# Optimization experiments

Measured on AMD Instinct MI355X. Metric: run time of the kernel, lower is better.

The kernel has to match this reference:

```python
import jax, jax.numpy as jnp
import numpy as np

NUM_HEADS = 8


def setup_inputs() -> dict:
    key = jax.random.key(0)
    ks = jax.random.split(key, 9)
    B, T, N, D = 8, 12, 307, 512
    scale = 0.02
    return {
        "query": jax.random.normal(ks[0], (B, T, N, D), dtype=jnp.float32),
        "key": jax.random.normal(ks[1], (B, T, N, D), dtype=jnp.float32),
        "value": jax.random.normal(ks[2], (B, T, N, D), dtype=jnp.float32),
        "semantic_matrix": jax.random.normal(ks[3], (N, N), dtype=jnp.float32),
        "Wq": jax.random.normal(ks[4], (D, D), dtype=jnp.float32) * scale,
        "bq": jnp.zeros((D,), dtype=jnp.float32),
        "Wk": jax.random.normal(ks[5], (D, D), dtype=jnp.float32) * scale,
        "bk": jnp.zeros((D,), dtype=jnp.float32),
        "Wv": jax.random.normal(ks[6], (D, D), dtype=jnp.float32) * scale,
        "bv": jnp.zeros((D,), dtype=jnp.float32),
        "Wo": jax.random.normal(ks[7], (D, D), dtype=jnp.float32) * scale,
        "bo": jnp.zeros((D,), dtype=jnp.float32),
    }


def reference(query, key, value, semantic_matrix, Wq, bq, Wk, bk, Wv, bv, Wo, bo):
    B, T, N, D = query.shape
    H = NUM_HEADS
    hd = D // H
    # multiplicative spatial mask: row-softmax of the semantic matrix (same for all b, h, t)
    mask = jax.nn.softmax(semantic_matrix, axis=-1)  # [N, N]
    q = (query @ Wq + bq).reshape(B, T, N, H, hd)
    k = (key @ Wk + bk).reshape(B, T, N, H, hd)
    v = (value @ Wv + bv).reshape(B, T, N, H, hd)
    # attention over the node axis, per (batch, head, time step)
    scores = jnp.einsum("btnhd,btmhd->bhtnm", q, k) * (1.0 / (hd ** 0.5))  # [B,H,T,N,N]
    scores = scores * mask  # elementwise multiplicative mask (NOT additive bias)
    w = jax.nn.softmax(scores, axis=-1)
    out = jnp.einsum("bhtnm,btmhd->btnhd", w, v).reshape(B, T, N, D)
    return out @ Wo + bo
```

## Files before the change

kernel.cpp:

```cpp
#include <hip/hip_runtime.h>

#define NNODES 307
#define NPAD 320
#define HEADS 8
#define HDV 64
#define DM 512
#define BATCH 8
#define TSTEPS 12
#define MROWS (BATCH*TSTEPS*NNODES)

typedef unsigned short u16;
typedef __attribute__((ext_vector_type(8))) short s16x8;
typedef __attribute__((ext_vector_type(8))) unsigned short u16x8;
typedef __attribute__((ext_vector_type(4))) float f32x4;

__device__ __forceinline__ u16 f2bf(float f){
  unsigned int u = __builtin_bit_cast(unsigned int, f);
  u += 0x7fffu + ((u >> 16) & 1u);
  return (u16)(u >> 16);
}
__device__ __forceinline__ unsigned f2bf2(float lo, float hi){
  return (unsigned)f2bf(lo) | ((unsigned)f2bf(hi) << 16);
}
__device__ __forceinline__ void glds16(const void* g, void* l){
  __builtin_amdgcn_global_load_lds((const __attribute__((address_space(1))) void*)g,
                                   (__attribute__((address_space(3))) void*)l, 16, 0, 0);
}

struct PrepArgs { const float* w[4]; u16* o[4]; };

__global__ __launch_bounds__(256)
void prep_w(PrepArgs a){
  const float* w = a.w[blockIdx.z];
  u16* o = a.o[blockIdx.z];
  __shared__ float tile[32][33];
  int bx = blockIdx.x*32, by = blockIdx.y*32;
  int tx = threadIdx.x, ty = threadIdx.y;
  for (int i = ty; i < 32; i += 8)
    tile[i][tx] = w[(size_t)(by+i)*DM + bx + tx];
  __syncthreads();
  for (int i = ty; i < 32; i += 8)
    o[(size_t)(bx+i)*DM + by + tx] = f2bf(tile[tx][i]);
}

__global__ __launch_bounds__(256)
void mask_softmax(const float* __restrict__ sem, float* __restrict__ maskp){
  int n = blockIdx.x;
  int tid = threadIdx.x, lane = tid & 63, wid = tid >> 6;
  if (n >= NNODES){
    maskp[(size_t)n*NPAD + tid] = 0.f;
    if (tid + 256 < NPAD) maskp[(size_t)n*NPAD + tid + 256] = 0.f;
    return;
  }
  __shared__ float red[4];
  float v0 = sem[(size_t)n*NNODES + tid];
  float v1 = (tid + 256 < NNODES) ? sem[(size_t)n*NNODES + tid + 256] : -INFINITY;
  float mx = fmaxf(v0, v1);
  for (int d = 1; d < 64; d <<= 1) mx = fmaxf(mx, __shfl_xor(mx, d));
  if (lane == 0) red[wid] = mx;
  __syncthreads();
  mx = fmaxf(fmaxf(red[0], red[1]), fmaxf(red[2], red[3]));
  __syncthreads();
  float e0 = __expf(v0 - mx);
  float e1 = (tid + 256 < NNODES) ? __expf(v1 - mx) : 0.f;
  float s = e0 + e1;
  for (int d = 1; d < 64; d <<= 1) s += __shfl_xor(s, d);
  if (lane == 0) red[wid] = s;
  __syncthreads();
  s = red[0] + red[1] + red[2] + red[3];
  float rs = 0.125f / s;
  maskp[(size_t)n*NPAD + tid] = e0 * rs;
  int c2 = tid + 256;
  if (c2 < NNODES)      maskp[(size_t)n*NPAD + c2] = e1 * rs;
  else if (c2 < NPAD)   maskp[(size_t)n*NPAD + c2] = 0.f;
}

struct GemmSet { const void* A; const u16* W; const float* bias; void* C; };
struct GemmArgs { GemmSet s[3]; };

template<int AF32, int CBF16>
__global__ __launch_bounds__(256)
void gemm512(GemmArgs ga, int M){
  GemmSet g = ga.s[blockIdx.y];
  __shared__ u16 As[128*64];
  __shared__ u16 Bs[128*64];
  const int tid = threadIdx.x;
  const int lane = tid & 63;
  const int wid = tid >> 6;

  int bid = blockIdx.x;
  const int qch = 924 >> 3, rch = 924 & 7;
  int xcd = bid & 7, idx = bid >> 3;
  int wg = (xcd < rch ? xcd*(qch+1) : rch*(qch+1) + (xcd-rch)*qch) + idx;
  const int m0 = (wg >> 2) * 128;
  const int n0 = (wg & 3) * 128;
  const int wr = (wid >> 1) * 64;
  const int wc = (wid & 1) * 64;

  const f32x4 fz = {0.f, 0.f, 0.f, 0.f};
  f32x4 acc[4][4];
#pragma unroll
  for (int i = 0; i < 4; i++)
#pragma unroll
    for (int j = 0; j < 4; j++) acc[i][j] = fz;

  const int rL = (wid << 5) + (lane >> 3);
  const int cswz = (lane & 7) ^ (rL & 7);
  const u16* bsrc = g.W + (size_t)(n0 + rL)*DM + cswz*8;
  const u16* asrcB = AF32 ? nullptr : ((const u16*)g.A + (size_t)(m0 + rL)*DM + cswz*8);

  const int sr = tid >> 1;
  const int shf = tid & 1;
  const int grA = m0 + sr;
  const bool okA = grA < M;

  for (int k0 = 0; k0 < 512; k0 += 64) {
#pragma unroll
    for (int e = 0; e < 4; e++)
      glds16(bsrc + (size_t)e*8*DM + k0, Bs + (wid << 11) + (e << 9));
    if constexpr (AF32) {
      const float* src = (const float*)g.A + (size_t)grA*DM + k0 + shf*32;
      u16x8 ch[4];
#pragma unroll
      for (int i = 0; i < 4; i++) {
        float4 f0 = okA ? ((const float4*)src)[2*i]   : make_float4(0.f,0.f,0.f,0.f);
        float4 f1 = okA ? ((const float4*)src)[2*i+1] : make_float4(0.f,0.f,0.f,0.f);
        u16x8 u;
        u[0]=f2bf(f0.x); u[1]=f2bf(f0.y); u[2]=f2bf(f0.z); u[3]=f2bf(f0.w);
        u[4]=f2bf(f1.x); u[5]=f2bf(f1.y); u[6]=f2bf(f1.z); u[7]=f2bf(f1.w);
        ch[i] = u;
      }
#pragma unroll
      for (int i = 0; i < 4; i++) {
        int slot = (shf*64 + i*16) ^ ((sr & 7) << 4);
        *(u16x8*)((char*)As + sr*128 + slot) = ch[i];
      }
    } else {
#pragma unroll
      for (int e = 0; e < 4; e++)
        glds16(asrcB + (size_t)e*8*DM + k0, As + (wid << 11) + (e << 9));
    }
    __syncthreads();
    __builtin_amdgcn_s_setprio(1);
#pragma unroll
    for (int kt = 0; kt < 2; kt++) {
      int kbyte = kt*64 + (lane >> 4)*16;
      s16x8 a[4], b[4];
#pragma unroll
      for (int i = 0; i < 4; i++) {
        int row = wr + i*16 + (lane & 15);
        a[i] = *(const s16x8*)((const char*)As + row*128 + (kbyte ^ ((row & 7) << 4)));
      }
#pragma unroll
      for (int j = 0; j < 4; j++) {
        int row = wc + j*16 + (lane & 15);
        b[j] = *(const s16x8*)((const char*)Bs + row*128 + (kbyte ^ ((row & 7) << 4)));
      }
#pragma unroll
      for (int i = 0; i < 4; i++)
#pragma unroll
        for (int j = 0; j < 4; j++)
          acc[i][j] = __builtin_amdgcn_mfma_f32_16x16x32_bf16(a[i], b[j], acc[i][j], 0, 0, 0);
    }
    __builtin_amdgcn_s_setprio(0);
    __syncthreads();
  }

#pragma unroll
  for (int j = 0; j < 4; j++) {
    int gcol = n0 + wc + j*16 + (lane & 15);
    float bv = g.bias[gcol];
#pragma unroll
    for (int i = 0; i < 4; i++) {
#pragma unroll
      for (int r = 0; r < 4; r++) {
        int grow = m0 + wr + i*16 + (lane >> 4)*4 + r;
        if (grow < M) {
          float v = acc[i][j][r] + bv;
          if constexpr (CBF16) ((u16*)g.C)[(size_t)grow*DM + gcol] = f2bf(v);
          else                 ((float*)g.C)[(size_t)grow*DM + gcol] = v;
        }
      }
    }
  }
}

__global__ __launch_bounds__(640, 3)
void attn_kernel(const u16* __restrict__ Qb, const u16* __restrict__ Kb,
                 const u16* __restrict__ Vb, const float* __restrict__ maskp,
                 u16* __restrict__ attnb){
  __shared__ u16 kw[NPAD*64];
  __shared__ u16 vt[64*NPAD];
  __shared__ u16 pb[10*2*16*40];
  const int tid = threadIdx.x;
  const int lane = tid & 63;
  const int wid = tid >> 6;
  const int qq = lane & 15;
  const int gg = lane >> 4;
  const int bth = blockIdx.x;
  const int h   = bth & 7;
  const int bt  = bth >> 3;
  const size_t base = (size_t)bt * NNODES;

  const u16x8 zu = {0,0,0,0,0,0,0,0};
  const s16x8 zs = {0,0,0,0,0,0,0,0};
  const f32x4 fz = {0.f,0.f,0.f,0.f};

  s16x8 qf[2][2];
#pragma unroll
  for (int s = 0; s < 2; s++) {
    int qt = wid*2 + s;
    int qrow = qt*16 + qq;
    if (qrow < NNODES) {
      const u16* qp = Qb + (base + qrow)*DM + h*HDV + gg*8;
      qf[s][0] = *(const s16x8*)(qp);
      qf[s][1] = *(const s16x8*)(qp + 32);
    } else { qf[s][0] = zs; qf[s][1] = zs; }
  }

  for (int i = tid; i < NPAD*8; i += 640) {
    int r = i >> 3, c = i & 7;
    u16x8 kv = zu, vv = zu;
    if (r < NNODES) {
      kv = *(const u16x8*)(Kb + (base + r)*DM + h*HDV + c*8);
      vv = *(const u16x8*)(Vb + (base + r)*DM + h*HDV + c*8);
    }
    *(u16x8*)((char*)kw + r*128 + ((c*16) ^ ((r & 7) << 4))) = kv;
#pragma unroll
    for (int j = 0; j < 8; j++) {
      int d = c*8 + j;
      *(u16*)((char*)vt + d*640 + ((r*2) ^ ((d & 7) << 4))) = vv[j];
    }
  }
  __syncthreads();

  u16* pbw = pb + wid*1280;

#pragma unroll
  for (int s = 0; s < 2; s++) {
    const int qt = wid*2 + s;
    const int n = qt*16 + qq;

    f32x4 sc[20];
#pragma unroll
    for (int t = 0; t < 20; t++) sc[t] = fz;
    __builtin_amdgcn_s_setprio(1);
#pragma unroll
    for (int t = 0; t < 20; t++) {
      int m = t*16 + qq;
#pragma unroll
      for (int kt = 0; kt < 2; kt++) {
        s16x8 kf = *(const s16x8*)((const char*)kw + m*128 + ((kt*64 + gg*16) ^ ((m & 7) << 4)));
        sc[t] = __builtin_amdgcn_mfma_f32_16x16x32_bf16(kf, qf[s][kt], sc[t], 0, 0, 0);
      }
    }
    __builtin_amdgcn_s_setprio(0);

    const float* mrow = maskp + (size_t)n*NPAD + gg*4;
#pragma unroll
    for (int t = 0; t < 20; t++) {
      float4 mk = *(const float4*)(mrow + t*16);
      sc[t][0] *= mk.x; sc[t][1] *= mk.y; sc[t][2] *= mk.z; sc[t][3] *= mk.w;
    }
#pragma unroll
    for (int r = 0; r < 4; r++)
      if (304 + gg*4 + r >= NNODES) sc[19][r] = -1e30f;

    float mx = -1e30f;
#pragma unroll
    for (int t = 0; t < 20; t++)
      mx = fmaxf(fmaxf(fmaxf(mx, sc[t][0]), fmaxf(sc[t][1], sc[t][2])), sc[t][3]);
    mx = fmaxf(mx, __shfl_xor(mx, 16));
    mx = fmaxf(mx, __shfl_xor(mx, 32));

    float sum = 0.f;
#pragma unroll
    for (int t = 0; t < 20; t++) {
#pragma unroll
      for (int r = 0; r < 4; r++) { float e = __expf(sc[t][r] - mx); sc[t][r] = e; sum += e; }
    }
    sum += __shfl_xor(sum, 16);
    sum += __shfl_xor(sum, 32);
    const float rinv = 1.f / sum;

    f32x4 o[4];
#pragma unroll
    for (int dt = 0; dt < 4; dt++) o[dt] = fz;
#pragma unroll
    for (int kt = 0; kt < 10; kt++) {
      u16* ps = pbw + (kt & 1)*640;
      uint2 w0, w1;
      w0.x = f2bf2(sc[2*kt][0]*rinv,   sc[2*kt][1]*rinv);
      w0.y = f2bf2(sc[2*kt][2]*rinv,   sc[2*kt][3]*rinv);
      w1.x = f2bf2(sc[2*kt+1][0]*rinv, sc[2*kt+1][1]*rinv);
      w1.y = f2bf2(sc[2*kt+1][2]*rinv, sc[2*kt+1][3]*rinv);
      *(uint2*)(ps + qq*40 + gg*4)      = w0;
      *(uint2*)(ps + qq*40 + 16 + gg*4) = w1;
      s16x8 pa = *(const s16x8*)(ps + qq*40 + gg*8);
      __builtin_amdgcn_s_setprio(1);
#pragma unroll
      for (int dt = 0; dt < 4; dt++) {
        int d = dt*16 + qq;
        s16x8 vb = *(const s16x8*)((const char*)vt + d*640 + ((kt*64 + gg*16) ^ ((d & 7) << 4)));
        o[dt] = __builtin_amdgcn_mfma_f32_16x16x32_bf16(pa, vb, o[dt], 0, 0, 0);
      }
      __builtin_amdgcn_s_setprio(0);
    }

#pragma unroll
    for (int dt = 0; dt < 4; dt++) {
#pragma unroll
      for (int r = 0; r < 4; r++) {
        int nn = qt*16 + gg*4 + r;
        if (nn < NNODES)
          attnb[(base + nn)*DM + h*HDV + dt*16 + qq] = f2bf(o[dt][r]);
      }
    }
  }
}

extern "C" void kernel_launch(void* const* d_in, const int* in_sizes, int n_in,
                              void* d_out, int out_size, void* d_ws, size_t ws_size,
                              hipStream_t stream) {
  const float* query = (const float*)d_in[0];
  const float* key   = (const float*)d_in[1];
  const float* value = (const float*)d_in[2];
  const float* sem   = (const float*)d_in[3];
  const float* Wq = (const float*)d_in[4];
  const float* bq = (const float*)d_in[5];
  const float* Wk = (const float*)d_in[6];
  const float* bk = (const float*)d_in[7];
  const float* Wv = (const float*)d_in[8];
  const float* bv = (const float*)d_in[9];
  const float* Wo = (const float*)d_in[10];
  const float* bo = (const float*)d_in[11];
  float* out = (float*)d_out;

  char* ws = (char*)d_ws;
  size_t off = 0;
  auto alloc = [&](size_t b) { size_t o = off; off += (b + 255) & ~(size_t)255; return o; };
  float* maskp = (float*)(ws + alloc((size_t)NPAD*NPAD*4));
  u16* wtq = (u16*)(ws + alloc((size_t)DM*DM*2));
  u16* wtk = (u16*)(ws + alloc((size_t)DM*DM*2));
  u16* wtv = (u16*)(ws + alloc((size_t)DM*DM*2));
  u16* wto = (u16*)(ws + alloc((size_t)DM*DM*2));
  u16* ab = (u16*)(ws + alloc((size_t)MROWS*DM*2));
  u16* qb = (u16*)(ws + alloc((size_t)MROWS*DM*2));
  u16* kb = (u16*)(ws + alloc((size_t)MROWS*DM*2));
  u16* vb = (u16*)(ws + alloc((size_t)MROWS*DM*2));
  if (off > ws_size) return;

  PrepArgs pa;
  pa.w[0] = Wq; pa.w[1] = Wk; pa.w[2] = Wv; pa.w[3] = Wo;
  pa.o[0] = wtq; pa.o[1] = wtk; pa.o[2] = wtv; pa.o[3] = wto;
  prep_w<<<dim3(16,16,4), dim3(32,8,1), 0, stream>>>(pa);

  mask_softmax<<<dim3(NPAD), dim3(256), 0, stream>>>(sem, maskp);

  GemmArgs g3;
  g3.s[0] = { query, wtq, bq, qb };
  g3.s[1] = { key,   wtk, bk, kb };
  g3.s[2] = { value, wtv, bv, vb };
  gemm512<1,1><<<dim3(924, 3), dim3(256), 0, stream>>>(g3, MROWS);

  attn_kernel<<<dim3(BATCH*TSTEPS*HEADS), dim3(640), 0, stream>>>(qb, kb, vb, maskp, ab);

  GemmArgs g1;
  g1.s[0] = { ab, wto, bo, out };
  g1.s[1] = g1.s[0];
  g1.s[2] = g1.s[0];
  gemm512<0,0><<<dim3(924, 1), dim3(256), 0, stream>>>(g1, MROWS);
}
```

Before: 509.5 us.

## Double-buffer GEMM K loop, stage bf16 epilogue via LDS, split attention into query-tile blocks

```diff
diff --git a/kernel.cpp b/kernel.cpp
--- a/kernel.cpp
+++ b/kernel.cpp
@@ -82,11 +82,11 @@
 __global__ __launch_bounds__(256)
 void gemm512(GemmArgs ga, int M){
   GemmSet g = ga.s[blockIdx.y];
-  __shared__ u16 As[128*64];
-  __shared__ u16 Bs[128*64];
+  __shared__ u16 lds[32768];
   const int tid = threadIdx.x;
   const int lane = tid & 63;
   const int wid = tid >> 6;
+  const int qq = lane & 15, gg = lane >> 4;
 
   int bid = blockIdx.x;
   const int qch = 924 >> 3, rch = 924 & 7;
@@ -107,54 +107,60 @@
   const int rL = (wid << 5) + (lane >> 3);
   const int cswz = (lane & 7) ^ (rL & 7);
   const u16* bsrc = g.W + (size_t)(n0 + rL)*DM + cswz*8;
-  const u16* asrcB = AF32 ? nullptr : ((const u16*)g.A + (size_t)(m0 + rL)*DM + cswz*8);
+  const u16* asrcB = (const u16*)g.A + (size_t)(m0 + rL)*DM + cswz*8;
+  const int ldst = (wid << 11);
 
   const int sr = tid >> 1;
   const int shf = tid & 1;
-  const int grA = m0 + sr;
-  const bool okA = grA < M;
-
-  for (int k0 = 0; k0 < 512; k0 += 64) {
+  const float* aptr = (const float*)g.A + (size_t)(m0 + sr)*DM + shf*32;
+  const bool okA = (m0 + sr) < M;
+
+  auto stageB = [&](int c, int k0){
+    u16* dst = lds + c*16384 + 8192 + ldst;
 #pragma unroll
     for (int e = 0; e < 4; e++)
-      glds16(bsrc + (size_t)e*8*DM + k0, Bs + (wid << 11) + (e << 9));
-    if constexpr (AF32) {
-      const float* src = (const float*)g.A + (size_t)grA*DM + k0 + shf*32;
-      u16x8 ch[4];
+      glds16(bsrc + (size_t)(e*8)*DM + k0, dst + (e << 9));
+  };
+  auto stageAg = [&](int c, int k0){
+    u16* dst = lds + c*16384 + ldst;
+#pragma unroll
+    for (int e = 0; e < 4; e++)
+      glds16(asrcB + (size_t)(e*8)*DM + k0, dst + (e << 9));
+  };
+  auto loadA = [&](float4* An, int k0){
+#pragma unroll
+    for (int i = 0; i < 8; i++)
+      An[i] = okA ? ((const float4*)(aptr + k0))[i] : make_float4(0.f,0.f,0.f,0.f);
+  };
+  auto writeA = [&](const float4* An, int c){
+    u16* Abuf = lds + c*16384;
+#pragma unroll
+    for (int i = 0; i < 4; i++) {
+      float4 f0 = An[2*i], f1 = An[2*i+1];
+      u16x8 u;
+      u[0]=f2bf(f0.x); u[1]=f2bf(f0.y); u[2]=f2bf(f0.z); u[3]=f2bf(f0.w);
+      u[4]=f2bf(f1.x); u[5]=f2bf(f1.y); u[6]=f2bf(f1.z); u[7]=f2bf(f1.w);
+      int slot = (shf*64 + i*16) ^ ((sr & 7) << 4);
+      *(u16x8*)((char*)Abuf + sr*128 + slot) = u;
+    }
+  };
+  auto compute = [&](int c){
+    const char* Abuf = (const char*)(lds + c*16384);
+    const char* Bbuf = Abuf + 16384;
+    __builtin_amdgcn_s_setprio(1);
+#pragma unroll
+    for (int kt = 0; kt < 2; kt++) {
+      int kbyte = kt*64 + gg*16;
+      s16x8 a[4], b[4];
 #pragma unroll
       for (int i = 0; i < 4; i++) {
-        float4 f0 = okA ? ((const float4*)src)[2*i]   : make_float4(0.f,0.f,0.f,0.f);
-        float4 f1 = okA ? ((const float4*)src)[2*i+1] : make_float4(0.f,0.f,0.f,0.f);
-        u16x8 u;
-        u[0]=f2bf(f0.x); u[1]=f2bf(f0.y); u[2]=f2bf(f0.z); u[3]=f2bf(f0.w);
-        u[4]=f2bf(f1.x); u[5]=f2bf(f1.y); u[6]=f2bf(f1.z); u[7]=f2bf(f1.w);
-        ch[i] = u;
-      }
-#pragma unroll
-      for (int i = 0; i < 4; i++) {
-        int slot = (shf*64 + i*16) ^ ((sr & 7) << 4);
-        *(u16x8*)((char*)As + sr*128 + slot) = ch[i];
-      }
-    } else {
-#pragma unroll
-      for (int e = 0; e < 4; e++)
-        glds16(asrcB + (size_t)e*8*DM + k0, As + (wid << 11) + (e << 9));
-    }
-    __syncthreads();
-    __builtin_amdgcn_s_setprio(1);
-#pragma unroll
-    for (int kt = 0; kt < 2; kt++) {
-      int kbyte = kt*64 + (lane >> 4)*16;
-      s16x8 a[4], b[4];
-#pragma unroll
-      for (int i = 0; i < 4; i++) {
-        int row = wr + i*16 + (lane & 15);
-        a[i] = *(const s16x8*)((const char*)As + row*128 + (kbyte ^ ((row & 7) << 4)));
+        int row = wr + i*16 + qq;
+        a[i] = *(const s16x8*)(Abuf + row*128 + (kbyte ^ ((row & 7) << 4)));
       }
 #pragma unroll
       for (int j = 0; j < 4; j++) {
-        int row = wc + j*16 + (lane & 15);
-        b[j] = *(const s16x8*)((const char*)Bs + row*128 + (kbyte ^ ((row & 7) << 4)));
+        int row = wc + j*16 + qq;
+        b[j] = *(const s16x8*)(Bbuf + row*128 + (kbyte ^ ((row & 7) << 4)));
       }
 #pragma unroll
       for (int i = 0; i < 4; i++)
@@ -163,158 +169,204 @@
           acc[i][j] = __builtin_amdgcn_mfma_f32_16x16x32_bf16(a[i], b[j], acc[i][j], 0, 0, 0);
     }
     __builtin_amdgcn_s_setprio(0);
+  };
+
+  float4 An[8];
+  if constexpr (AF32) { loadA(An, 0); stageB(0, 0); writeA(An, 0); }
+  else { stageAg(0, 0); stageB(0, 0); }
+  __syncthreads();
+
+#pragma unroll
+  for (int t = 0; t < 8; t++) {
+    const int cur = t & 1;
+    if (t < 7) {
+      if constexpr (AF32) loadA(An, (t+1)*64);
+      else stageAg(cur^1, (t+1)*64);
+      stageB(cur^1, (t+1)*64);
+    }
+    compute(cur);
+    if constexpr (AF32) { if (t < 7) writeA(An, cur^1); }
     __syncthreads();
   }
 
-#pragma unroll
-  for (int j = 0; j < 4; j++) {
-    int gcol = n0 + wc + j*16 + (lane & 15);
-    float bv = g.bias[gcol];
-#pragma unroll
-    for (int i = 0; i < 4; i++) {
-#pragma unroll
-      for (int r = 0; r < 4; r++) {
-        int grow = m0 + wr + i*16 + (lane >> 4)*4 + r;
-        if (grow < M) {
-          float v = acc[i][j][r] + bv;
-          if constexpr (CBF16) ((u16*)g.C)[(size_t)grow*DM + gcol] = f2bf(v);
-          else                 ((float*)g.C)[(size_t)grow*DM + gcol] = v;
+  if constexpr (CBF16) {
+    u16* ct = lds;
+#pragma unroll
+    for (int j = 0; j < 4; j++) {
+      float bv = g.bias[n0 + wc + j*16 + qq];
+#pragma unroll
+      for (int i = 0; i < 4; i++)
+#pragma unroll
+        for (int r = 0; r < 4; r++)
+          ct[(wr + i*16 + gg*4 + r)*136 + wc + j*16 + qq] = f2bf(acc[i][j][r] + bv);
+    }
+    __syncthreads();
+#pragma unroll
+    for (int it = 0; it < 8; it++) {
+      int i = tid + it*256;
+      int row = i >> 4, seg = i & 15;
+      if (m0 + row < M)
+        *(u16x8*)((u16*)g.C + (size_t)(m0+row)*DM + n0 + seg*8) =
+            *(const u16x8*)(ct + row*136 + seg*8);
+    }
+  } else {
+#pragma unroll
+    for (int j = 0; j < 4; j++) {
+      int gcol = n0 + wc + j*16 + qq;
+      float bv = g.bias[gcol];
+#pragma unroll
+      for (int i = 0; i < 4; i++)
+#pragma unroll
+        for (int r = 0; r < 4; r++) {
+          int grow = m0 + wr + i*16 + gg*4 + r;
+          if (grow < M) ((float*)g.C)[(size_t)grow*DM + gcol] = acc[i][j][r] + bv;
         }
-      }
     }
   }
 }
 
-__global__ __launch_bounds__(640, 3)
+__global__ __launch_bounds__(256, 3)
 void attn_kernel(const u16* __restrict__ Qb, const u16* __restrict__ Kb,
                  const u16* __restrict__ Vb, const float* __restrict__ maskp,
                  u16* __restrict__ attnb){
-  __shared__ u16 kw[NPAD*64];
-  __shared__ u16 vt[64*NPAD];
-  __shared__ u16 pb[10*2*16*40];
+  __shared__ u16 kw[160*64];
+  __shared__ u16 vt[64*192];
+  __shared__ u16 pb[4*16*40];
   const int tid = threadIdx.x;
   const int lane = tid & 63;
   const int wid = tid >> 6;
   const int qq = lane & 15;
   const int gg = lane >> 4;
-  const int bth = blockIdx.x;
+  const int qt = blockIdx.x * 4 + wid;
+  const int bth = blockIdx.y;
   const int h   = bth & 7;
   const int bt  = bth >> 3;
   const size_t base = (size_t)bt * NNODES;
+  const int n = qt*16 + qq;
 
   const u16x8 zu = {0,0,0,0,0,0,0,0};
   const s16x8 zs = {0,0,0,0,0,0,0,0};
   const f32x4 fz = {0.f,0.f,0.f,0.f};
 
-  s16x8 qf[2][2];
-#pragma unroll
-  for (int s = 0; s < 2; s++) {
-    int qt = wid*2 + s;
-    int qrow = qt*16 + qq;
-    if (qrow < NNODES) {
-      const u16* qp = Qb + (base + qrow)*DM + h*HDV + gg*8;
-      qf[s][0] = *(const s16x8*)(qp);
-      qf[s][1] = *(const s16x8*)(qp + 32);
-    } else { qf[s][0] = zs; qf[s][1] = zs; }
-  }
-
-  for (int i = tid; i < NPAD*8; i += 640) {
-    int r = i >> 3, c = i & 7;
-    u16x8 kv = zu, vv = zu;
-    if (r < NNODES) {
-      kv = *(const u16x8*)(Kb + (base + r)*DM + h*HDV + c*8);
-      vv = *(const u16x8*)(Vb + (base + r)*DM + h*HDV + c*8);
-    }
-    *(u16x8*)((char*)kw + r*128 + ((c*16) ^ ((r & 7) << 4))) = kv;
-#pragma unroll
-    for (int j = 0; j < 8; j++) {
-      int d = c*8 + j;
-      *(u16*)((char*)vt + d*640 + ((r*2) ^ ((d & 7) << 4))) = vv[j];
-    }
-  }
-  __syncthreads();
-
-  u16* pbw = pb + wid*1280;
-
-#pragma unroll
-  for (int s = 0; s < 2; s++) {
-    const int qt = wid*2 + s;
-    const int n = qt*16 + qq;
-
-    f32x4 sc[20];
-#pragma unroll
-    for (int t = 0; t < 20; t++) sc[t] = fz;
+  s16x8 qf[2];
+  if (n < NNODES) {
+    const u16* qp = Qb + (base + n)*DM + h*HDV + gg*8;
+    qf[0] = *(const s16x8*)(qp);
+    qf[1] = *(const s16x8*)(qp + 32);
+  } else { qf[0] = zs; qf[1] = zs; }
+
+  f32x4 o[4] = {fz, fz, fz, fz};
+  float m_run = -1e30f, l_run = 0.f;
+  u16* pbw = pb + wid*640;
+
+  for (int hf = 0; hf < 2; hf++) {
+    for (int i = tid; i < 160*8; i += 256) {
+      int rl = i >> 3, c = i & 7, gr = hf*160 + rl;
+      u16x8 kv = zu, vv = zu;
+      if (gr < NNODES) {
+        kv = *(const u16x8*)(Kb + (base + gr)*DM + h*HDV + c*8);
+        vv = *(const u16x8*)(Vb + (base + gr)*DM + h*HDV + c*8);
+      }
+      *(u16x8*)((char*)kw + rl*128 + ((c*16) ^ ((rl & 7) << 4))) = kv;
+#pragma unroll
+      for (int j = 0; j < 8; j++) {
+        int d = c*8 + j;
+        *(u16*)((char*)vt + d*384 + ((rl*2) ^ ((d & 7) << 4))) = vv[j];
+      }
+    }
+    __syncthreads();
+
+    f32x4 sc[10];
+#pragma unroll
+    for (int t = 0; t < 10; t++) sc[t] = fz;
     __builtin_amdgcn_s_setprio(1);
 #pragma unroll
-    for (int t = 0; t < 20; t++) {
-      int m = t*16 + qq;
+    for (int t = 0; t < 10; t++) {
+      int ml = t*16 + qq;
 #pragma unroll
       for (int kt = 0; kt < 2; kt++) {
-        s16x8 kf = *(const s16x8*)((const char*)kw + m*128 + ((kt*64 + gg*16) ^ ((m & 7) << 4)));
-        sc[t] = __builtin_amdgcn_mfma_f32_16x16x32_bf16(kf, qf[s][kt], sc[t], 0, 0, 0);
+        s16x8 kf = *(const s16x8*)((const char*)kw + ml*128 + ((kt*64 + gg*16) ^ ((ml & 7) << 4)));
+        sc[t] = __builtin_amdgcn_mfma_f32_16x16x32_bf16(kf, qf[kt], sc[t], 0, 0, 0);
       }
     }
     __builtin_amdgcn_s_setprio(0);
 
-    const float* mrow = maskp + (size_t)n*NPAD + gg*4;
-#pragma unroll
-    for (int t = 0; t < 20; t++) {
+    const float* mrow = maskp + (size_t)n*NPAD + hf*160 + gg*4;
+#pragma unroll
+    for (int t = 0; t < 10; t++) {
       float4 mk = *(const float4*)(mrow + t*16);
       sc[t][0] *= mk.x; sc[t][1] *= mk.y; sc[t][2] *= mk.z; sc[t][3] *= mk.w;
     }
-#pragma unroll
-    for (int r = 0; r < 4; r++)
-      if (304 + gg*4 + r >= NNODES) sc[19][r] = -1e30f;
-
-    float mx = -1e30f;
-#pragma unroll
-    for (int t = 0; t < 20; t++)
-      mx = fmaxf(fmaxf(fmaxf(mx, sc[t][0]), fmaxf(sc[t][1], sc[t][2])), sc[t][3]);
-    mx = fmaxf(mx, __shfl_xor(mx, 16));
-    mx = fmaxf(mx, __shfl_xor(mx, 32));
-
+    if (hf) {
+#pragma unroll
+      for (int r = 0; r < 4; r++)
+        if (304 + gg*4 + r >= NNODES) sc[9][r] = -1e30f;
+    }
+
+    float mh = -1e30f;
+#pragma unroll
+    for (int t = 0; t < 10; t++)
+      mh = fmaxf(fmaxf(fmaxf(mh, sc[t][0]), fmaxf(sc[t][1], sc[t][2])), sc[t][3]);
+    mh = fmaxf(mh, __shfl_xor(mh, 16));
+    mh = fmaxf(mh, __shfl_xor(mh, 32));
+    float mnew = fmaxf(m_run, mh);
+    float scl = __expf(m_run - mnew);
+    m_run = mnew;
     float sum = 0.f;
 #pragma unroll
-    for (int t = 0; t < 20; t++) {
-#pragma unroll
-      for (int r = 0; r < 4; r++) { float e = __expf(sc[t][r] - mx); sc[t][r] = e; sum += e; }
+    for (int t = 0; t < 10; t++) {
+#pragma unroll
+      for (int r = 0; r < 4; r++) { float e = __expf(sc[t][r] - mnew); sc[t][r] = e; sum += e; }
     }
     sum += __shfl_xor(sum, 16);
     sum += __shfl_xor(sum, 32);
-    const float rinv = 1.f / sum;
-
-    f32x4 o[4];
-#pragma unroll
-    for (int dt = 0; dt < 4; dt++) o[dt] = fz;
-#pragma unroll
-    for (int kt = 0; kt < 10; kt++) {
-      u16* ps = pbw + (kt & 1)*640;
+    l_run = l_run * scl + sum;
+    float srs[4];
+#pragma unroll
+    for (int r = 0; r < 4; r++) srs[r] = __shfl(scl, gg*4 + r);
+#pragma unroll
+    for (int dt = 0; dt < 4; dt++) {
+      o[dt][0] *= srs[0]; o[dt][1] *= srs[1]; o[dt][2] *= srs[2]; o[dt][3] *= srs[3];
+    }
+
+#pragma unroll
+    for (int kt = 0; kt < 5; kt++) {
       uint2 w0, w1;
-      w0.x = f2bf2(sc[2*kt][0]*rinv,   sc[2*kt][1]*rinv);
-      w0.y = f2bf2(sc[2*kt][2]*rinv,   sc[2*kt][3]*rinv);
-      w1.x = f2bf2(sc[2*kt+1][0]*rinv, sc[2*kt+1][1]*rinv);
-      w1.y = f2bf2(sc[2*kt+1][2]*rinv, sc[2*kt+1][3]*rinv);
-      *(uint2*)(ps + qq*40 + gg*4)      = w0;
-      *(uint2*)(ps + qq*40 + 16 + gg*4) = w1;
-      s16x8 pa = *(const s16x8*)(ps + qq*40 + gg*8);
+      w0.x = f2bf2(sc[2*kt][0],   sc[2*kt][1]);
+      w0.y = f2bf2(sc[2*kt][2],   sc[2*kt][3]);
+      w1.x = f2bf2(sc[2*kt+1][0], sc[2*kt+1][1]);
+      w1.y = f2bf2(sc[2*kt+1][2], sc[2*kt+1][3]);
+      *(uint2*)(pbw + qq*40 + gg*4)      = w0;
+      *(uint2*)(pbw + qq*40 + 16 + gg*4) = w1;
+      s16x8 pa = *(const s16x8*)(pbw + qq*40 + gg*8);
       __builtin_amdgcn_s_setprio(1);
 #pragma unroll
       for (int dt = 0; dt < 4; dt++) {
         int d = dt*16 + qq;
-        s16x8 vb = *(const s16x8*)((const char*)vt + d*640 + ((kt*64 + gg*16) ^ ((d & 7) << 4)));
-        o[dt] = __builtin_amdgcn_mfma_f32_16x16x32_bf16(pa, vb, o[dt], 0, 0, 0);
+        s16x8 vbf = *(const s16x8*)((const char*)vt + d*384 + ((kt*64 + gg*16) ^ ((d & 7) << 4)));
+        o[dt] = __builtin_amdgcn_mfma_f32_16x16x32_bf16(pa, vbf, o[dt], 0, 0, 0);
       }
       __builtin_amdgcn_s_setprio(0);
     }
-
-#pragma unroll
-    for (int dt = 0; dt < 4; dt++) {
-#pragma unroll
-      for (int r = 0; r < 4; r++) {
-        int nn = qt*16 + gg*4 + r;
-        if (nn < NNODES)
-          attnb[(base + nn)*DM + h*HDV + dt*16 + qq] = f2bf(o[dt][r]);
-      }
+    __syncthreads();
+  }
+
+  float li[4];
+#pragma unroll
+  for (int r = 0; r < 4; r++) li[r] = 1.f / __shfl(l_run, gg*4 + r);
+  u16* ow = kw + wid*1152;
+#pragma unroll
+  for (int dt = 0; dt < 4; dt++)
+#pragma unroll
+    for (int r = 0; r < 4; r++)
+      ow[(gg*4 + r)*72 + dt*16 + qq] = f2bf(o[dt][r] * li[r]);
+  {
+    int row = lane >> 2, segb = (lane & 3)*16;
+    int nn = qt*16 + row;
+    if (nn < NNODES) {
+      u16* dst = attnb + (base + nn)*DM + h*HDV + segb;
+      *(u16x8*)(dst)     = *(const u16x8*)(ow + row*72 + segb);
+      *(u16x8*)(dst + 8) = *(const u16x8*)(ow + row*72 + segb + 8);
     }
   }
 }
@@ -363,7 +415,7 @@
   g3.s[2] = { value, wtv, bv, vb };
   gemm512<1,1><<<dim3(924, 3), dim3(256), 0, stream>>>(g3, MROWS);
 
-  attn_kernel<<<dim3(BATCH*TSTEPS*HEADS), dim3(640), 0, stream>>>(qb, kb, vb, maskp, ab);
+  attn_kernel<<<dim3(5, BATCH*TSTEPS*HEADS), dim3(256), 0, stream>>>(qb, kb, vb, maskp, ab);
 
   GemmArgs g1;
   g1.s[0] = { ab, wto, bo, out };
```

Result: faster. 445.0 us (-12.7%).
